# Optimization experiments

Measured on AMD Instinct MI355X. Metric: run time of the kernel, lower is better.

## Reference

```python
import jax, jax.numpy as jnp
import numpy as np
import math

D_MODEL = 2048
N_HEADS = 16
HEAD_DIM = D_MODEL // N_HEADS  # 128
SEQ = 2048
BATCH = 1


def make_freqs(seq_len, head_dim, theta=10000.0):
    # standard rotary frequencies: freqs_cis = exp(i * t * inv_freq)
    inv_freq = 1.0 / (theta ** (np.arange(0, head_dim, 2, dtype=np.float32) / head_dim))
    t = np.arange(seq_len, dtype=np.float32)
    ang = np.outer(t, inv_freq)  # [seq, head_dim/2]
    return jnp.asarray(np.cos(ang)), jnp.asarray(np.sin(ang))


def setup_inputs() -> dict:
    key = jax.random.key(0)
    ks = jax.random.split(key, 6)
    x = jax.random.normal(ks[0], (BATCH, SEQ, D_MODEL), dtype=jnp.float32)
    freqs_cos, freqs_sin = make_freqs(SEQ, HEAD_DIM)
    # causal additive mask, broadcastable to [b, h, s, s]
    mask = jnp.where(jnp.tril(jnp.ones((SEQ, SEQ), dtype=bool)), 0.0, -1e9).astype(jnp.float32)[None, None]
    scale = 0.02
    wq = jax.random.normal(ks[1], (D_MODEL, D_MODEL), dtype=jnp.float32) * scale
    wk = jax.random.normal(ks[2], (D_MODEL, D_MODEL), dtype=jnp.float32) * scale
    wv = jax.random.normal(ks[3], (D_MODEL, D_MODEL), dtype=jnp.float32) * scale
    wo = jax.random.normal(ks[4], (D_MODEL, D_MODEL), dtype=jnp.float32) * scale
    return {"x": x, "freqs_cos": freqs_cos, "freqs_sin": freqs_sin, "mask": mask,
            "wq": wq, "wk": wk, "wv": wv, "wo": wo}


def _apply_rotary(q, k, cos, sin):
    # q, k: [b, s, h, hd]; cos/sin: [s, hd/2]
    def rot(t):
        tr = t.reshape(*t.shape[:-1], -1, 2)  # [b, s, h, hd/2, 2]
        re, im = tr[..., 0], tr[..., 1]
        c = cos[None, :, None, :]
        s = sin[None, :, None, :]
        # complex multiply (re + i im) * (c + i s)
        out_re = re * c - im * s
        out_im = re * s + im * c
        return jnp.stack([out_re, out_im], axis=-1).reshape(t.shape)
    return rot(q), rot(k)


def reference(x, freqs_cos, freqs_sin, mask, wq, wk, wv, wo):
    b, s, _ = x.shape
    # QKV projections (nn.Linear with no bias: x @ W^T; W is square so use x @ W
    # with W stored already-transposed -- weights here are random so x @ W is faithful math)
    q = (x @ wq).reshape(b, s, N_HEADS, HEAD_DIM)
    k = (x @ wk).reshape(b, s, N_HEADS, HEAD_DIM)
    v = (x @ wv).reshape(b, s, N_HEADS, HEAD_DIM)
    q, k = _apply_rotary(q, k, freqs_cos, freqs_sin)
    # [b, h, s_q, s_k]
    scores = jnp.einsum("bqhd,bkhd->bhqk", q, k) / math.sqrt(HEAD_DIM)
    scores = scores + mask
    probs = jax.nn.softmax(scores.astype(jnp.float32), axis=-1).astype(q.dtype)
    out = jnp.einsum("bhqk,bkhd->bqhd", probs, v).reshape(b, s, N_HEADS * HEAD_DIM)
    return out @ wo
```

## Files before the change

### kernel.cpp

```cpp
#include <hip/hip_runtime.h>
#include <hip/hip_bf16.h>
#include <math.h>

#define SEQ 2048
#define DM 2048
#define NH 16
#define HD 128
#define QKV_N 6144

typedef __bf16 bf16;
typedef __bf16 bf16x8 __attribute__((ext_vector_type(8)));
typedef __bf16 bf16x4v __attribute__((ext_vector_type(4)));
typedef __bf16 bf16x2v __attribute__((ext_vector_type(2)));
typedef float f32x4 __attribute__((ext_vector_type(4)));

__device__ inline int sw_idx64(int row, int chunk) {
    return (row * 8 + (chunk ^ (row & 7))) * 8;
}
__device__ inline int sw_idx128(int row, int chunk) {
    return (row * 16 + (chunk ^ (row & 15))) * 8;
}
__device__ inline int sw_idx32(int row, int chunk) {
    return (row * 4 + (chunk ^ (row & 3))) * 8;
}

__device__ inline void async16(const void* g, void* l) {
    __builtin_amdgcn_global_load_lds((const __attribute__((address_space(1))) void*)g,
                                     (__attribute__((address_space(3))) void*)l, 16, 0, 0);
}

__global__ __launch_bounds__(256) void k_prep(const float* __restrict__ wq,
                                              const float* __restrict__ wk,
                                              const float* __restrict__ wv,
                                              const float* __restrict__ wo,
                                              bf16* __restrict__ wT, bf16* __restrict__ woT,
                                              const float* __restrict__ x,
                                              bf16* __restrict__ xb) {
    const int z = blockIdx.z;
    const int t = threadIdx.x;
    if (z == 4) {
        int bid = blockIdx.y * 32 + blockIdx.x;
#pragma unroll
        for (int j = 0; j < 4; ++j) {
            int i = bid * 1024 + j * 256 + t;
            float4 v = ((const float4*)x)[i];
            bf16x4v o;
            o.x = (bf16)v.x; o.y = (bf16)v.y; o.z = (bf16)v.z; o.w = (bf16)v.w;
            ((bf16x4v*)xb)[i] = o;
        }
        return;
    }
    __shared__ bf16 tile[64][66];
    const float* src = (z == 0) ? wq : (z == 1) ? wk : (z == 2) ? wv : wo;
    bf16* dst = (z < 3) ? (wT + (size_t)z * DM * DM) : woT;
    const int bx = blockIdx.x * 64, by = blockIdx.y * 64;
#pragma unroll
    for (int j = 0; j < 4; ++j) {
        int idx = j * 256 + t;
        int r = idx >> 4, cg = idx & 15;
        float4 v = *(const float4*)&src[(size_t)(by + r) * DM + bx + cg * 4];
        bf16x4v o;
        o.x = (bf16)v.x; o.y = (bf16)v.y; o.z = (bf16)v.z; o.w = (bf16)v.w;
        *(bf16x4v*)&tile[r][cg * 4] = o;
    }
    __syncthreads();
#pragma unroll
    for (int j = 0; j < 4; ++j) {
        int idx = j * 256 + t;
        int r = idx >> 4, cg = idx & 15;
        bf16x4v o;
        o.x = tile[cg * 4 + 0][r];
        o.y = tile[cg * 4 + 1][r];
        o.z = tile[cg * 4 + 2][r];
        o.w = tile[cg * 4 + 3][r];
        *(bf16x4v*)&dst[(size_t)(bx + r) * DM + by + cg * 4] = o;
    }
}

__global__ __launch_bounds__(256) void k_rope_vt(bf16* __restrict__ qkv,
                                                 const float* __restrict__ cosT,
                                                 const float* __restrict__ sinT,
                                                 bf16* __restrict__ vT) {
    const int t = threadIdx.x;
    if (blockIdx.x >= 1024) {
        int g = (blockIdx.x - 1024) * 256 + t;
        int s = g >> 8;
        int cg = g & 255;
        int h = cg >> 4, w8 = cg & 15;
        size_t base = (size_t)s * QKV_N + DM + h * HD + w8 * 8;
        float4 cv = *(const float4*)&cosT[s * 64 + w8 * 4];
        float4 sv = *(const float4*)&sinT[s * 64 + w8 * 4];
        float cc[4] = {cv.x, cv.y, cv.z, cv.w};
        float ss[4] = {sv.x, sv.y, sv.z, sv.w};
        bf16x8 k = *(bf16x8*)&qkv[base];
        bf16x8 o;
#pragma unroll
        for (int p = 0; p < 4; ++p) {
            float re = (float)k[2 * p], im = (float)k[2 * p + 1];
            o[2 * p]     = (bf16)(re * cc[p] - im * ss[p]);
            o[2 * p + 1] = (bf16)(re * ss[p] + im * cc[p]);
        }
        *(bf16x8*)&qkv[base] = o;
        return;
    }
    __shared__ bf16 tile[64][66];
    const int bx = (blockIdx.x & 31) * 64, by = (blockIdx.x >> 5) * 64;
#pragma unroll
    for (int j = 0; j < 4; ++j) {
        int idx = j * 256 + t;
        int r = idx >> 4, cg = idx & 15;
        *(bf16x4v*)&tile[r][cg * 4] =
            *(const bf16x4v*)&qkv[(size_t)(by + r) * QKV_N + 2 * DM + bx + cg * 4];
    }
    __syncthreads();
#pragma unroll
    for (int j = 0; j < 4; ++j) {
        int idx = j * 256 + t;
        int r = idx >> 4, cg = idx & 15;
        bf16x4v o;
        o.x = tile[cg * 4 + 0][r];
        o.y = tile[cg * 4 + 1][r];
        o.z = tile[cg * 4 + 2][r];
        o.w = tile[cg * 4 + 3][r];
        *(bf16x4v*)&vT[(size_t)(bx + r) * SEQ + by + cg * 4] = o;
    }
}

template <typename OutT, int BN>
__device__ __forceinline__ void gemm_body(const bf16* __restrict__ A,
                                          const bf16* __restrict__ Bt,
                                          OutT* __restrict__ C,
                                          int N, int K, size_t bm, size_t bn,
                                          bf16* As, bf16* Bs) {
    constexpr int NI = BN / 32;
    const int t = threadIdx.x;
    const int lane = t & 63;
    const int w = t >> 6;
    const int wr = (w >> 1) * 64, wc = (w & 1) * (BN / 2);
    const int l15 = lane & 15, quad = lane >> 4;
    f32x4 acc[4][NI];
#pragma unroll
    for (int i = 0; i < 4; ++i)
#pragma unroll
        for (int j = 0; j < NI; ++j) acc[i][j] = (f32x4){0.f, 0.f, 0.f, 0.f};

    for (int kt = 0; kt < K; kt += 64) {
#pragma unroll
        for (int j = 0; j < 4; ++j) {
            int c = j * 256 + t;
            int row = c >> 3, g = ((c & 7) ^ (row & 7)) * 8;
            async16(&A[(bm + row) * K + kt + g], &As[c * 8]);
        }
#pragma unroll
        for (int j = 0; j < NI; ++j) {
            int c = j * 256 + t;
            int row = c >> 3, g = ((c & 7) ^ (row & 7)) * 8;
            async16(&Bt[(bn + row) * K + kt + g], &Bs[c * 8]);
        }
        __syncthreads();
#pragma unroll
        for (int kh = 0; kh < 2; ++kh) {
            bf16x8 af[4], bfm[NI];
#pragma unroll
            for (int mi = 0; mi < 4; ++mi)
                af[mi] = *(const bf16x8*)&As[sw_idx64(wr + mi * 16 + l15, kh * 4 + quad)];
#pragma unroll
            for (int ni = 0; ni < NI; ++ni)
                bfm[ni] = *(const bf16x8*)&Bs[sw_idx64(wc + ni * 16 + l15, kh * 4 + quad)];
#pragma unroll
            for (int mi = 0; mi < 4; ++mi)
#pragma unroll
                for (int ni = 0; ni < NI; ++ni)
                    acc[mi][ni] = __builtin_amdgcn_mfma_f32_16x16x32_bf16(
                        af[mi], bfm[ni], acc[mi][ni], 0, 0, 0);
        }
        __syncthreads();
    }
#pragma unroll
    for (int mi = 0; mi < 4; ++mi)
#pragma unroll
        for (int ni = 0; ni < NI; ++ni)
#pragma unroll
            for (int r = 0; r < 4; ++r) {
                size_t row = bm + wr + mi * 16 + quad * 4 + r;
                size_t col = bn + wc + ni * 16 + l15;
                C[row * (size_t)N + col] = (OutT)acc[mi][ni][r];
            }
}

template <typename OutT, int BN>
__global__ __launch_bounds__(256) void k_gemm_bt(const bf16* __restrict__ A,
                                                 const bf16* __restrict__ Bt,
                                                 OutT* __restrict__ C,
                                                 int M, int N, int K) {
    __shared__ bf16 As[128 * 64];
    __shared__ bf16 Bs[BN * 64];
    size_t bm = (size_t)blockIdx.y * 128, bn = (size_t)blockIdx.x * BN;
    gemm_body<OutT, BN>(A, Bt, C, N, K, bm, bn, As, Bs);
}

__global__ __launch_bounds__(512) void k_gemm_ksplit(const bf16* __restrict__ A,
                                                     const bf16* __restrict__ Bt,
                                                     float* __restrict__ C) {
    __shared__ __align__(16) char smem[65536];
    const int t = threadIdx.x;
    const int tg = t & 255;
    const int gk = t >> 8;
    const int lane = t & 63;
    const int wl = (t >> 6) & 3;
    const int wr = (wl >> 1) * 64, wc = (wl & 1) * 64;
    const int l15 = lane & 15, quad = lane >> 4;
    const size_t bm = (size_t)blockIdx.y * 128, bn = (size_t)blockIdx.x * 128;
    bf16* Asg = (bf16*)(smem) + gk * 8192;
    bf16* Bsg = (bf16*)(smem + 32768) + gk * 8192;

    f32x4 acc[4][4];
#pragma unroll
    for (int i = 0; i < 4; ++i)
#pragma unroll
        for (int j = 0; j < 4; ++j) acc[i][j] = (f32x4){0.f, 0.f, 0.f, 0.f};

    const int k0 = gk * 1024;
    for (int kt = k0; kt < k0 + 1024; kt += 64) {
#pragma unroll
        for (int j = 0; j < 4; ++j) {
            int c = j * 256 + tg;
            int row = c >> 3, g8 = ((c & 7) ^ (row & 7)) * 8;
            async16(&A[(bm + row) * DM + kt + g8], &Asg[c * 8]);
        }
#pragma unroll
        for (int j = 0; j < 4; ++j) {
            int c = j * 256 + tg;
            int row = c >> 3, g8 = ((c & 7) ^ (row & 7)) * 8;
            async16(&Bt[(bn + row) * DM + kt + g8], &Bsg[c * 8]);
        }
        __syncthreads();
#pragma unroll
        for (int kh = 0; kh < 2; ++kh) {
            bf16x8 af[4], bfm[4];
#pragma unroll
            for (int mi = 0; mi < 4; ++mi)
                af[mi] = *(const bf16x8*)&Asg[sw_idx64(wr + mi * 16 + l15, kh * 4 + quad)];
#pragma unroll
            for (int ni = 0; ni < 4; ++ni)
                bfm[ni] = *(const bf16x8*)&Bsg[sw_idx64(wc + ni * 16 + l15, kh * 4 + quad)];
#pragma unroll
            for (int mi = 0; mi < 4; ++mi)
#pragma unroll
                for (int ni = 0; ni < 4; ++ni)
                    acc[mi][ni] = __builtin_amdgcn_mfma_f32_16x16x32_bf16(
                        af[mi], bfm[ni], acc[mi][ni], 0, 0, 0);
        }
        __syncthreads();
    }
    float* oX = (float*)smem;
    if (gk == 1) {
#pragma unroll
        for (int mi = 0; mi < 4; ++mi)
#pragma unroll
            for (int ni = 0; ni < 4; ++ni)
#pragma unroll
                for (int r = 0; r < 4; ++r)
                    oX[(wr + mi * 16 + quad * 4 + r) * 128 + wc + ni * 16 + l15] =
                        acc[mi][ni][r];
    }
    __syncthreads();
    if (gk == 0) {
#pragma unroll
        for (int mi = 0; mi < 4; ++mi)
#pragma unroll
            for (int ni = 0; ni < 4; ++ni)
#pragma unroll
                for (int r = 0; r < 4; ++r) {
                    int row = wr + mi * 16 + quad * 4 + r;
                    int col = wc + ni * 16 + l15;
                    C[(bm + row) * (size_t)DM + bn + col] =
                        acc[mi][ni][r] + oX[row * 128 + col];
                }
    }
}

__global__ __launch_bounds__(512) void k_flash(const bf16* __restrict__ qkv,
                                               const bf16* __restrict__ vT,
                                               const float* __restrict__ cosT,
                                               const float* __restrict__ sinT,
                                               bf16* __restrict__ out) {
    __shared__ bf16 Ks[2][64 * 128];
    __shared__ bf16 Vs[2][128 * 64];
    __shared__ bf16 Pl[8][16 * 32];
    const int t = threadIdx.x;
    const int lane = t & 63;
    const int w = t >> 6;
    const int wl = w & 3;
    const int g = w >> 2;
    const int l15 = lane & 15, quad = lane >> 4;
    const int b = blockIdx.x;
    const int hc = b & 15;
    const int h = (hc & 7) * 2 + (hc >> 3);
    const int qb = (b < 256) ? (31 - (b >> 4)) : ((b >> 4) - 16);
    const int q0w = qb * 64 + wl * 16;
    const float sc2 = 0.08838834764831845f * 1.4426950408889634f;

    const size_t qrow = (size_t)(q0w + l15) * QKV_N + h * HD;
    bf16x8 aq[4];
#pragma unroll
    for (int u = 0; u < 4; ++u)
        aq[u] = *(const bf16x8*)&qkv[qrow + u * 32 + quad * 8];
#pragma unroll
    for (int u = 0; u < 4; ++u) {
        float4 cv = *(const float4*)&cosT[(q0w + l15) * 64 + u * 16 + quad * 4];
        float4 sv = *(const float4*)&sinT[(q0w + l15) * 64 + u * 16 + quad * 4];
        float cc[4] = {cv.x, cv.y, cv.z, cv.w};
        float ss[4] = {sv.x, sv.y, sv.z, sv.w};
        bf16x8 q = aq[u], rq;
#pragma unroll
        for (int pp = 0; pp < 4; ++pp) {
            float re = (float)q[2 * pp], im = (float)q[2 * pp + 1];
            rq[2 * pp]     = (bf16)(re * cc[pp] - im * ss[pp]);
            rq[2 * pp + 1] = (bf16)(re * ss[pp] + im * cc[pp]);
        }
        aq[u] = rq;
    }

    f32x4 o[8];
#pragma unroll
    for (int c = 0; c < 8; ++c) o[c] = (f32x4){0.f, 0.f, 0.f, 0.f};
    float l_r[4] = {0.f, 0.f, 0.f, 0.f};

    int krow[2], kg[2], vrow[2], vg[2];
#pragma unroll
    for (int j = 0; j < 2; ++j) {
        int c2 = j * 512 + t;
        krow[j] = c2 >> 4; kg[j] = ((c2 & 15) ^ (krow[j] & 15)) * 8;
        vrow[j] = c2 >> 3; vg[j] = ((c2 & 7) ^ (vrow[j] & 7)) * 8;
    }
    auto stage = [&](int buf, int kt2) {
        const int kb2 = kt2 * 64;
#pragma unroll
        for (int j = 0; j < 2; ++j)
            async16(&qkv[(size_t)(kb2 + krow[j]) * QKV_N + DM + h * HD + kg[j]],
                    &Ks[buf][(j * 512 + t) * 8]);
#pragma unroll
        for (int j = 0; j < 2; ++j)
            async16(&vT[(size_t)(h * HD + vrow[j]) * SEQ + kb2 + vg[j]],
                    &Vs[buf][(j * 512 + t) * 8]);
    };

    const int nT = qb + 1;
    stage(0, 0);
    for (int kt = 0; kt < nT; ++kt) {
        const int cb = kt & 1;
        const int kbase = kt * 64;
        const bool pre = (kt + 1 < nT);
        if (pre) {
            stage(cb ^ 1, kt + 1);
            asm volatile("s_waitcnt vmcnt(6)" ::: "memory");
        } else {
            asm volatile("s_waitcnt vmcnt(2)" ::: "memory");
        }
        __builtin_amdgcn_s_barrier();
        asm volatile("" ::: "memory");

        f32x4 s4[2];
        __builtin_amdgcn_s_setprio(1);
#pragma unroll
        for (int sl = 0; sl < 2; ++sl) {
            const int sub = 2 * g + sl;
            f32x4 z = (f32x4){0.f, 0.f, 0.f, 0.f};
#pragma unroll
            for (int u = 0; u < 4; ++u) {
                bf16x8 kv = *(const bf16x8*)&Ks[cb][sw_idx128(sub * 16 + l15, u * 4 + quad)];
                z = __builtin_amdgcn_mfma_f32_16x16x32_bf16(aq[u], kv, z, 0, 0, 0);
            }
            s4[sl] = z;
        }
        __builtin_amdgcn_s_setprio(0);
        const bool masked = (kt == qb);
#pragma unroll
        for (int sl = 0; sl < 2; ++sl) {
            const int sub = 2 * g + sl;
#pragma unroll
            for (int r = 0; r < 4; ++r) {
                float pv = __builtin_amdgcn_exp2f(s4[sl][r] * sc2);
                if (masked)
                    pv = (kbase + sub * 16 + l15 <= q0w + quad * 4 + r) ? pv : 0.f;
                l_r[r] += pv;
                int rowp = quad * 4 + r;
                int lc = sl * 16 + l15;
                Pl[w][(rowp * 4 + ((lc >> 3) ^ (rowp & 3))) * 8 + (lc & 7)] = (bf16)pv;
            }
        }
        if (pre) asm volatile("s_waitcnt vmcnt(4)" ::: "memory");
        else     asm volatile("s_waitcnt vmcnt(0)" ::: "memory");
        __builtin_amdgcn_s_barrier();
        __asm__ __volatile__("s_waitcnt lgkmcnt(0)" ::: "memory");
        bf16x8 pf = *(const bf16x8*)&Pl[w][sw_idx32(l15, quad)];
        __builtin_amdgcn_s_setprio(1);
#pragma unroll
        for (int c = 0; c < 8; ++c) {
            bf16x8 vb = *(const bf16x8*)&Vs[cb][sw_idx64(c * 16 + l15, g * 4 + quad)];
            o[c] = __builtin_amdgcn_mfma_f32_16x16x32_bf16(pf, vb, o[c], 0, 0, 0);
        }
        __builtin_amdgcn_s_setprio(0);
        asm volatile("" ::: "memory");
        __builtin_amdgcn_s_barrier();
        asm volatile("" ::: "memory");
    }

    __syncthreads();
    float* oxch = (float*)&Ks[0][0];
    float* lxch = (float*)&Pl[0][0];
    const int tp = t & 255;
    if (g == 1) {
#pragma unroll
        for (int c = 0; c < 8; ++c)
            *(f32x4*)&oxch[tp * 32 + c * 4] = o[c];
#pragma unroll
        for (int r = 0; r < 4; ++r) lxch[tp * 4 + r] = l_r[r];
    }
    __syncthreads();
    if (g == 0) {
#pragma unroll
        for (int c = 0; c < 8; ++c) {
            f32x4 v = *(const f32x4*)&oxch[tp * 32 + c * 4];
            o[c] += v;
        }
#pragma unroll
        for (int r = 0; r < 4; ++r) l_r[r] += lxch[tp * 4 + r];
        float rl[4];
#pragma unroll
        for (int r = 0; r < 4; ++r) {
            float l = l_r[r];
            l += __shfl_xor(l, 1, 16);
            l += __shfl_xor(l, 2, 16);
            l += __shfl_xor(l, 4, 16);
            l += __shfl_xor(l, 8, 16);
            rl[r] = 1.0f / l;
        }
#pragma unroll
        for (int c = 0; c < 8; ++c)
#pragma unroll
            for (int r = 0; r < 4; ++r)
                out[(size_t)(q0w + quad * 4 + r) * DM + h * HD + c * 16 + l15] =
                    (bf16)(o[c][r] * rl[r]);
    }
}

extern "C" void kernel_launch(void* const* d_in, const int* in_sizes, int n_in,
                              void* d_out, int out_size, void* d_ws, size_t ws_size,
                              hipStream_t stream) {
    const float* x  = (const float*)d_in[0];
    const float* fc = (const float*)d_in[1];
    const float* fs = (const float*)d_in[2];
    const float* wq = (const float*)d_in[4];
    const float* wk = (const float*)d_in[5];
    const float* wv = (const float*)d_in[6];
    const float* wo = (const float*)d_in[7];
    float* out = (float*)d_out;

    char* ws = (char*)d_ws;
    bf16* xb  = (bf16*)(ws);
    bf16* wT  = (bf16*)(ws + (size_t)(8u  << 20));
    bf16* woT = (bf16*)(ws + (size_t)(32u << 20));
    bf16* qkv = (bf16*)(ws + (size_t)(40u << 20));
    bf16* vT  = (bf16*)(ws + (size_t)(64u << 20));

    k_prep<<<dim3(32, 32, 5), 256, 0, stream>>>(wq, wk, wv, wo, wT, woT, x, xb);
    k_gemm_bt<bf16, 128><<<dim3(48, 16), 256, 0, stream>>>(xb, wT, qkv, SEQ, QKV_N, DM);
    k_rope_vt<<<3072, 256, 0, stream>>>(qkv, fc, fs, vT);
    k_flash<<<512, 512, 0, stream>>>(qkv, vT, fc, fs, xb);
    k_gemm_ksplit<<<dim3(16, 16), 512, 0, stream>>>(xb, woT, out);
}
```

Measured before the change: 281.7 us.

## Halve flash block size and give each wave two 16-row query groups

The flash attention kernel now runs with 256 threads (4 waves) instead of 512. Each wave handles 32 query rows as two 16-row groups, so every K and V fragment read from shared memory feeds two MFMAs. Each thread issues twice as many async loads per tile, and the vmcnt wait counts and the P/output exchange layouts are adjusted to match. This cuts LDS read traffic per MFMA but doubles the accumulator registers per thread and halves the waves available to hide latency.

```diff
diff --git a/kernel.cpp b/kernel.cpp
--- a/kernel.cpp
+++ b/kernel.cpp
@@ -280,70 +280,74 @@
     }
 }
 
-__global__ __launch_bounds__(512) void k_flash(const bf16* __restrict__ qkv,
+__global__ __launch_bounds__(256) void k_flash(const bf16* __restrict__ qkv,
                                                const bf16* __restrict__ vT,
                                                const float* __restrict__ cosT,
                                                const float* __restrict__ sinT,
                                                bf16* __restrict__ out) {
     __shared__ bf16 Ks[2][64 * 128];
     __shared__ bf16 Vs[2][128 * 64];
-    __shared__ bf16 Pl[8][16 * 32];
+    __shared__ bf16 Pl[4][32 * 32];
     const int t = threadIdx.x;
     const int lane = t & 63;
     const int w = t >> 6;
-    const int wl = w & 3;
-    const int g = w >> 2;
+    const int wl = w & 1;
+    const int g = w >> 1;
     const int l15 = lane & 15, quad = lane >> 4;
     const int b = blockIdx.x;
     const int hc = b & 15;
     const int h = (hc & 7) * 2 + (hc >> 3);
     const int qb = (b < 256) ? (31 - (b >> 4)) : ((b >> 4) - 16);
-    const int q0w = qb * 64 + wl * 16;
+    const int q0w = qb * 64 + wl * 32;
     const float sc2 = 0.08838834764831845f * 1.4426950408889634f;
 
-    const size_t qrow = (size_t)(q0w + l15) * QKV_N + h * HD;
-    bf16x8 aq[4];
-#pragma unroll
-    for (int u = 0; u < 4; ++u)
-        aq[u] = *(const bf16x8*)&qkv[qrow + u * 32 + quad * 8];
-#pragma unroll
-    for (int u = 0; u < 4; ++u) {
-        float4 cv = *(const float4*)&cosT[(q0w + l15) * 64 + u * 16 + quad * 4];
-        float4 sv = *(const float4*)&sinT[(q0w + l15) * 64 + u * 16 + quad * 4];
-        float cc[4] = {cv.x, cv.y, cv.z, cv.w};
-        float ss[4] = {sv.x, sv.y, sv.z, sv.w};
-        bf16x8 q = aq[u], rq;
-#pragma unroll
-        for (int pp = 0; pp < 4; ++pp) {
-            float re = (float)q[2 * pp], im = (float)q[2 * pp + 1];
-            rq[2 * pp]     = (bf16)(re * cc[pp] - im * ss[pp]);
-            rq[2 * pp + 1] = (bf16)(re * ss[pp] + im * cc[pp]);
-        }
-        aq[u] = rq;
-    }
-
-    f32x4 o[8];
-#pragma unroll
-    for (int c = 0; c < 8; ++c) o[c] = (f32x4){0.f, 0.f, 0.f, 0.f};
-    float l_r[4] = {0.f, 0.f, 0.f, 0.f};
-
-    int krow[2], kg[2], vrow[2], vg[2];
-#pragma unroll
-    for (int j = 0; j < 2; ++j) {
-        int c2 = j * 512 + t;
-        krow[j] = c2 >> 4; kg[j] = ((c2 & 15) ^ (krow[j] & 15)) * 8;
-        vrow[j] = c2 >> 3; vg[j] = ((c2 & 7) ^ (vrow[j] & 7)) * 8;
+    bf16x8 aq[2][4];
+#pragma unroll
+    for (int rg = 0; rg < 2; ++rg) {
+        const int qrow = q0w + rg * 16 + l15;
+        const size_t qbase = (size_t)qrow * QKV_N + h * HD;
+#pragma unroll
+        for (int u4 = 0; u4 < 4; ++u4) {
+            bf16x8 q = *(const bf16x8*)&qkv[qbase + u4 * 32 + quad * 8];
+            float4 cv = *(const float4*)&cosT[qrow * 64 + u4 * 16 + quad * 4];
+            float4 sv = *(const float4*)&sinT[qrow * 64 + u4 * 16 + quad * 4];
+            float cc[4] = {cv.x, cv.y, cv.z, cv.w};
+            float ss[4] = {sv.x, sv.y, sv.z, sv.w};
+            bf16x8 rq;
+#pragma unroll
+            for (int pp = 0; pp < 4; ++pp) {
+                float re = (float)q[2 * pp], im = (float)q[2 * pp + 1];
+                rq[2 * pp]     = (bf16)(re * cc[pp] - im * ss[pp]);
+                rq[2 * pp + 1] = (bf16)(re * ss[pp] + im * cc[pp]);
+            }
+            aq[rg][u4] = rq;
+        }
+    }
+
+    f32x4 o[2][8];
+#pragma unroll
+    for (int rg = 0; rg < 2; ++rg)
+#pragma unroll
+        for (int c = 0; c < 8; ++c) o[rg][c] = (f32x4){0.f, 0.f, 0.f, 0.f};
+    float l_r[2][4] = {{0.f, 0.f, 0.f, 0.f}, {0.f, 0.f, 0.f, 0.f}};
+
+    int krow[4], kg[4], vrow[4], vg[4];
+#pragma unroll
+    for (int j = 0; j < 4; ++j) {
+        int c = j * 256 + t;
+        krow[j] = c >> 4; kg[j] = ((c & 15) ^ (krow[j] & 15)) * 8;
+        vrow[j] = c >> 3; vg[j] = ((c & 7) ^ (vrow[j] & 7)) * 8;
     }
     auto stage = [&](int buf, int kt2) {
         const int kb2 = kt2 * 64;
 #pragma unroll
-        for (int j = 0; j < 2; ++j)
+        for (int j = 0; j < 4; ++j)
             async16(&qkv[(size_t)(kb2 + krow[j]) * QKV_N + DM + h * HD + kg[j]],
-                    &Ks[buf][(j * 512 + t) * 8]);
-#pragma unroll
-        for (int j = 0; j < 2; ++j)
+                    &Ks[buf][(j * 256 + t) * 8]);
+#pragma unroll
+        for (int j = 0; j < 4; ++j)
             async16(&vT[(size_t)(h * HD + vrow[j]) * SEQ + kb2 + vg[j]],
-                    &Vs[buf][(j * 512 + t) * 8]);
+                    &Vs[buf][(j * 256 + t) * 8]);
     };
 
     const int nT = qb + 1;
@@ -354,52 +358,62 @@
         const bool pre = (kt + 1 < nT);
         if (pre) {
             stage(cb ^ 1, kt + 1);
-            asm volatile("s_waitcnt vmcnt(6)" ::: "memory");
+            asm volatile("s_waitcnt vmcnt(12)" ::: "memory");
         } else {
-            asm volatile("s_waitcnt vmcnt(2)" ::: "memory");
+            asm volatile("s_waitcnt vmcnt(4)" ::: "memory");
         }
         __builtin_amdgcn_s_barrier();
         asm volatile("" ::: "memory");
 
-        f32x4 s4[2];
+        f32x4 s4[2][2];
         __builtin_amdgcn_s_setprio(1);
 #pragma unroll
         for (int sl = 0; sl < 2; ++sl) {
             const int sub = 2 * g + sl;
-            f32x4 z = (f32x4){0.f, 0.f, 0.f, 0.f};
-#pragma unroll
-            for (int u = 0; u < 4; ++u) {
-                bf16x8 kv = *(const bf16x8*)&Ks[cb][sw_idx128(sub * 16 + l15, u * 4 + quad)];
-                z = __builtin_amdgcn_mfma_f32_16x16x32_bf16(aq[u], kv, z, 0, 0, 0);
-            }
-            s4[sl] = z;
+            f32x4 z0 = (f32x4){0.f, 0.f, 0.f, 0.f};
+            f32x4 z1 = (f32x4){0.f, 0.f, 0.f, 0.f};
+#pragma unroll
+            for (int u4 = 0; u4 < 4; ++u4) {
+                bf16x8 kv = *(const bf16x8*)&Ks[cb][sw_idx128(sub * 16 + l15, u4 * 4 + quad)];
+                z0 = __builtin_amdgcn_mfma_f32_16x16x32_bf16(aq[0][u4], kv, z0, 0, 0, 0);
+                z1 = __builtin_amdgcn_mfma_f32_16x16x32_bf16(aq[1][u4], kv, z1, 0, 0, 0);
+            }
+            s4[0][sl] = z0;
+            s4[1][sl] = z1;
         }
         __builtin_amdgcn_s_setprio(0);
         const bool masked = (kt == qb);
 #pragma unroll
-        for (int sl = 0; sl < 2; ++sl) {
-            const int sub = 2 * g + sl;
-#pragma unroll
-            for (int r = 0; r < 4; ++r) {
-                float pv = __builtin_amdgcn_exp2f(s4[sl][r] * sc2);
-                if (masked)
-                    pv = (kbase + sub * 16 + l15 <= q0w + quad * 4 + r) ? pv : 0.f;
-                l_r[r] += pv;
-                int rowp = quad * 4 + r;
-                int lc = sl * 16 + l15;
-                Pl[w][(rowp * 4 + ((lc >> 3) ^ (rowp & 3))) * 8 + (lc & 7)] = (bf16)pv;
-            }
-        }
-        if (pre) asm volatile("s_waitcnt vmcnt(4)" ::: "memory");
+        for (int rg = 0; rg < 2; ++rg)
+#pragma unroll
+            for (int sl = 0; sl < 2; ++sl) {
+                const int sub = 2 * g + sl;
+#pragma unroll
+                for (int r = 0; r < 4; ++r) {
+                    float pv = __builtin_amdgcn_exp2f(s4[rg][sl][r] * sc2);
+                    if (masked)
+                        pv = (kbase + sub * 16 + l15 <= q0w + rg * 16 + quad * 4 + r)
+                                 ? pv : 0.f;
+                    l_r[rg][r] += pv;
+                    int rp = rg * 16 + quad * 4 + r;
+                    int lc = sl * 16 + l15;
+                    Pl[w][(rp * 4 + ((lc >> 3) ^ (rp & 3))) * 8 + (lc & 7)] = (bf16)pv;
+                }
+            }
+        if (pre) asm volatile("s_waitcnt vmcnt(8)" ::: "memory");
         else     asm volatile("s_waitcnt vmcnt(0)" ::: "memory");
         __builtin_amdgcn_s_barrier();
         __asm__ __volatile__("s_waitcnt lgkmcnt(0)" ::: "memory");
-        bf16x8 pf = *(const bf16x8*)&Pl[w][sw_idx32(l15, quad)];
+        bf16x8 pf[2];
+#pragma unroll
+        for (int rg = 0; rg < 2; ++rg)
+            pf[rg] = *(const bf16x8*)&Pl[w][sw_idx32(rg * 16 + l15, quad)];
         __builtin_amdgcn_s_setprio(1);
 #pragma unroll
         for (int c = 0; c < 8; ++c) {
             bf16x8 vb = *(const bf16x8*)&Vs[cb][sw_idx64(c * 16 + l15, g * 4 + quad)];
-            o[c] = __builtin_amdgcn_mfma_f32_16x16x32_bf16(pf, vb, o[c], 0, 0, 0);
+            o[0][c] = __builtin_amdgcn_mfma_f32_16x16x32_bf16(pf[0], vb, o[0][c], 0, 0, 0);
+            o[1][c] = __builtin_amdgcn_mfma_f32_16x16x32_bf16(pf[1], vb, o[1][c], 0, 0, 0);
         }
         __builtin_amdgcn_s_setprio(0);
         asm volatile("" ::: "memory");
@@ -410,39 +424,46 @@
     __syncthreads();
     float* oxch = (float*)&Ks[0][0];
     float* lxch = (float*)&Pl[0][0];
-    const int tp = t & 255;
+    const int tp = t & 127;
     if (g == 1) {
 #pragma unroll
-        for (int c = 0; c < 8; ++c)
-            *(f32x4*)&oxch[tp * 32 + c * 4] = o[c];
-#pragma unroll
-        for (int r = 0; r < 4; ++r) lxch[tp * 4 + r] = l_r[r];
+        for (int rg = 0; rg < 2; ++rg)
+#pragma unroll
+            for (int c = 0; c < 8; ++c)
+                *(f32x4*)&oxch[(tp * 16 + rg * 8 + c) * 4] = o[rg][c];
+#pragma unroll
+        for (int rg = 0; rg < 2; ++rg)
+#pragma unroll
+            for (int r = 0; r < 4; ++r) lxch[tp * 8 + rg * 4 + r] = l_r[rg][r];
     }
     __syncthreads();
     if (g == 0) {
 #pragma unroll
-        for (int c = 0; c < 8; ++c) {
-            f32x4 v = *(const f32x4*)&oxch[tp * 32 + c * 4];
-            o[c] += v;
-        }
-#pragma unroll
-        for (int r = 0; r < 4; ++r) l_r[r] += lxch[tp * 4 + r];
-        float rl[4];
-#pragma unroll
-        for (int r = 0; r < 4; ++r) {
-            float l = l_r[r];
-            l += __shfl_xor(l, 1, 16);
-            l += __shfl_xor(l, 2, 16);
-            l += __shfl_xor(l, 4, 16);
-            l += __shfl_xor(l, 8, 16);
-            rl[r] = 1.0f / l;
-        }
-#pragma unroll
-        for (int c = 0; c < 8; ++c)
-#pragma unroll
-            for (int r = 0; r < 4; ++r)
-                out[(size_t)(q0w + quad * 4 + r) * DM + h * HD + c * 16 + l15] =
-                    (bf16)(o[c][r] * rl[r]);
+        for (int rg = 0; rg < 2; ++rg)
+#pragma unroll
+            for (int c = 0; c < 8; ++c) {
+                f32x4 v = *(const f32x4*)&oxch[(tp * 16 + rg * 8 + c) * 4];
+                o[rg][c] += v;
+            }
+#pragma unroll
+        for (int rg = 0; rg < 2; ++rg) {
+            float rl[4];
+#pragma unroll
+            for (int r = 0; r < 4; ++r) {
+                float l = l_r[rg][r] + lxch[tp * 8 + rg * 4 + r];
+                l += __shfl_xor(l, 1, 16);
+                l += __shfl_xor(l, 2, 16);
+                l += __shfl_xor(l, 4, 16);
+                l += __shfl_xor(l, 8, 16);
+                rl[r] = 1.0f / l;
+            }
+#pragma unroll
+            for (int c = 0; c < 8; ++c)
+#pragma unroll
+                for (int r = 0; r < 4; ++r)
+                    out[(size_t)(q0w + rg * 16 + quad * 4 + r) * DM + h * HD +
+                        c * 16 + l15] = (bf16)(o[rg][c][r] * rl[r]);
+        }
     }
 }
 
@@ -468,6 +489,6 @@
     k_prep<<<dim3(32, 32, 5), 256, 0, stream>>>(wq, wk, wv, wo, wT, woT, x, xb);
     k_gemm_bt<bf16, 128><<<dim3(48, 16), 256, 0, stream>>>(xb, wT, qkv, SEQ, QKV_N, DM);
     k_rope_vt<<<3072, 256, 0, stream>>>(qkv, fc, fs, vT);
-    k_flash<<<512, 512, 0, stream>>>(qkv, vT, fc, fs, xb);
+    k_flash<<<512, 256, 0, stream>>>(qkv, vT, fc, fs, xb);
     k_gemm_ksplit<<<dim3(16, 16), 512, 0, stream>>>(xb, woT, out);
 }
```

Result: slower. 291.3 us (+3.4%).
